# Optimization experiments

Hardware: AMD Instinct MI355X
Metric: run time of the kernel (lower is better)

Reference implementation:

```python
import jax, jax.numpy as jnp
import numpy as np

T_INF = 10
LR_R = 0.02
EPS = 1e-5

def conv(x, w):
    # torch F.conv2d, padding=1, OIHW weights, NCHW data
    return jax.lax.conv_general_dilated(x, w, (1, 1), ((1, 1), (1, 1)),
                                        dimension_numbers=('NCHW', 'OIHW', 'NCHW'))

def convT(x, w):
    # torch ConvTranspose2d (stride=1, padding=1), weight layout (Cin, Cout, kH, kW)
    # equivalent to conv with spatially-flipped, channel-swapped kernel
    wc = jnp.flip(w, (2, 3)).transpose(1, 0, 2, 3)
    return conv(x, wc)

def maxpool2(x):
    return jax.lax.reduce_window(x, -jnp.inf, jax.lax.max, (1, 1, 2, 2), (1, 1, 2, 2), 'VALID')

def avgpool2(x):
    return jax.lax.reduce_window(x, 0.0, jax.lax.add, (1, 1, 2, 2), (1, 1, 2, 2), 'VALID') * 0.25

def bn(x, g, b):
    # BatchNorm2d in training mode (batch statistics, biased variance), eps=1e-5
    m = x.mean((0, 2, 3), keepdims=True)
    v = x.var((0, 2, 3), keepdims=True)
    return (x - m) * jax.lax.rsqrt(v + EPS) * g[None, :, None, None] + b[None, :, None, None]

def up2(x):
    return jnp.repeat(jnp.repeat(x, 2, axis=2), 2, axis=3)

def setup_inputs() -> dict:
    key = jax.random.key(0)
    B, C1, C2, C3 = 256, 64, 128, 256
    ks = jax.random.split(key, 12)
    def w(k, shape, fan_in):
        return jax.random.normal(k, shape, jnp.float32) * (1.0 / np.sqrt(fan_in))
    return {
        'x':  jax.random.normal(ks[0], (B, 3, 32, 32), jnp.float32),
        'W1': w(ks[1], (C1, 3, 3, 3), 3 * 9),
        'W2': w(ks[2], (C2, C1, 3, 3), C1 * 9),
        'W3': w(ks[3], (C3, C2, 3, 3), C2 * 9),
        'P2': w(ks[4], (C2, C1, 3, 3), C2 * 9),  # ConvTranspose2d(C2, C1) weight layout
        'P3': w(ks[5], (C3, C2, 3, 3), C3 * 9),  # ConvTranspose2d(C3, C2) weight layout
        'g1': jnp.ones((C1,), jnp.float32), 'b1': jnp.zeros((C1,), jnp.float32),
        'g2': jnp.ones((C2,), jnp.float32), 'b2': jnp.zeros((C2,), jnp.float32),
        'g3': jnp.ones((C3,), jnp.float32), 'b3': jnp.zeros((C3,), jnp.float32),
    }

def reference(x, W1, W2, W3, P2, P3, g1, b1, g2, b2, g3, b3):
    # feed-forward initialization
    r1 = maxpool2(jax.nn.relu(bn(conv(x, W1), g1, b1)))   # [B,C1,16,16]
    r2 = maxpool2(jax.nn.relu(bn(conv(r1, W2), g2, b2)))  # [B,C2,8,8]
    r3 = maxpool2(jax.nn.relu(bn(conv(r2, W3), g3, b3)))  # [B,C3,4,4]
    # iterative predictive-coding inference
    for _ in range(T_INF):
        pred1 = jnp.tanh(up2(convT(r2, P2)))  # P2(r2) is 8x8, upsample to 16x16
        pred2 = jnp.tanh(up2(convT(r3, P3)))  # P3(r3) is 4x4, upsample to 8x8
        e1 = r1 - pred1
        e2 = r2 - pred2
        dr1 = -e1
        dr2 = -e2 + avgpool2(conv(e1, W2))
        dr3 = avgpool2(conv(e2, W3))
        r1 = jax.nn.relu(r1 + LR_R * dr1)
        r2 = jax.nn.relu(r2 + LR_R * dr2)
        r3 = jax.nn.relu(r3 + LR_R * dr3)
    return (r1, r2, r3)
```

## Files before the change

### kernel.cpp

```cpp
#include <hip/hip_runtime.h>
#include <cstddef>
#include <cstdint>

#define LRr 0.02f

typedef unsigned short u16;
typedef __attribute__((ext_vector_type(8))) __bf16 bf16x8;
typedef __attribute__((ext_vector_type(8))) short short8;
typedef __attribute__((ext_vector_type(4))) float f32x4;
typedef __attribute__((ext_vector_type(4))) u16 u16x4;

static __device__ __forceinline__ u16 f2bf(float f) {
  union { float f; unsigned int u; } v{f};
  unsigned int r = (v.u + 0x7FFFu + ((v.u >> 16) & 1u)) >> 16;
  return (u16)r;
}
static __device__ __forceinline__ float bf2f(u16 h) {
  union { unsigned int u; float f; } v{(unsigned int)h << 16};
  return v.f;
}

static __device__ __forceinline__ void gload_lds16(const void* g, void* l) {
  __builtin_amdgcn_global_load_lds(
      (const __attribute__((address_space(1))) unsigned int*)g,
      (__attribute__((address_space(3))) unsigned int*)l, 16, 0, 0);
}

enum { EP_RAW = 0, EP_E1 = 1, EP_E2 = 2, EP_P2 = 3, EP_P3 = 4 };

template<int H, int CIN, int COUT, int WAVES_M, int WAVES_N, int WN, int NBLK,
         int CS, int IMGS, int EPI, bool STATS>
__device__ __forceinline__ void gemm_body(
    int bid, char* lds,
    const u16* __restrict__ in, const u16* __restrict__ wpk,
    float* __restrict__ fout, u16* __restrict__ bout,
    const u16* __restrict__ aux, float* __restrict__ sums)
{
  constexpr int P = H * H, W = H;
  constexpr int LW = (H == 16) ? 4 : ((H == 8) ? 3 : 2);
  constexpr bool HALO = (IMGS == 1);
  constexpr int MROWS = IMGS * P;
  constexpr int WM = MROWS / WAVES_M;
  constexpr int M_rep = WM / 16, N_rep = WN / 16;
  constexpr int COB = WAVES_N * WN;
  constexpr int PW = H + 2;
  constexpr int ASZ = HALO ? PW * PW * CIN * 2 : MROWS * CIN * 2;
  constexpr int BCH = CS * COB * 2;
  constexpr int CH = CIN / CS;
  constexpr int NS = 9 * CH;
  constexpr int BR = (CS * COB) / 2048;
  static_assert(COB * NBLK == COUT, "n");
  static_assert(WAVES_M * WAVES_N == 4, "w");
  static_assert(ASZ + 2 * BCH <= 65536, "lds");
  static_assert((CS * COB) % 2048 == 0, "br");

  const int tid = threadIdx.x;
  const int l = tid & 63, l15 = l & 15, lq = l >> 4;
  const int wid = tid >> 6;
  const int wn = wid % WAVES_N, wm = wid / WAVES_N;
  const int img0 = (bid / NBLK) * IMGS;
  const int half = bid % NBLK;
  const int co0b = half * COB;
  const int wm0 = wm * WM;
  const int co = co0b + wn * WN;

  auto stageB = [&](int buf, int s) {
    int tap = s / CH, ch = s % CH;
#pragma unroll
    for (int r = 0; r < BR; ++r) {
      int j = r * 256 + tid;
      int ci8 = ch * (CS / 8) + j / COB, c = j % COB;
      const char* gp = (const char*)wpk +
          ((size_t)((tap * (CIN / 8) + ci8) * COUT + co0b + c) << 4);
      char* lp = lds + ASZ + buf * BCH + ((r * 256 + (tid & 192)) << 4);
      gload_lds16(gp, lp);
    }
  };

  stageB(0, 0);
  if constexpr (HALO) {
    for (int i = tid * 16; i < ASZ; i += 4096)
      *(int4*)(lds + i) = make_int4(0, 0, 0, 0);
    __syncthreads();
    constexpr int NCH = P * CIN / 8;
    for (int i = tid; i < NCH; i += 256) {
      int pix = i / (CIN / 8), c8 = i % (CIN / 8);
      const char* gp = (const char*)in + (((size_t)img0 * P + pix) * CIN + c8 * 8) * 2;
      int cell = ((pix >> LW) + 1) * PW + (pix & (W - 1)) + 1;
      int lb = ((cell * CIN + c8 * 8) << 1) ^ ((cell & 7) << 4);
      *(short8*)(lds + lb) = *(const short8*)gp;
    }
  } else {
    constexpr int NCH = MROWS * CIN / 8;
    for (int i = tid; i < NCH; i += 256) {
      int row = i / (CIN / 8), c8 = i % (CIN / 8);
      const char* gp = (const char*)in + ((size_t)img0 * P * CIN + (size_t)i * 8) * 2;
      int lb = ((row * CIN + c8 * 8) << 1) ^ ((row & 7) << 4);
      *(short8*)(lds + lb) = *(const short8*)gp;
    }
  }
  __syncthreads();

  f32x4 acc[M_rep][N_rep];
#pragma unroll
  for (int m = 0; m < M_rep; ++m)
#pragma unroll
    for (int n = 0; n < N_rep; ++n)
#pragma unroll
      for (int r = 0; r < 4; ++r) acc[m][n][r] = 0.f;

  int ym[M_rep], xm[M_rep], imb[M_rep];
#pragma unroll
  for (int m = 0; m < M_rep; ++m) {
    int rb = wm0 + m * 16;
    if constexpr (HALO) {
      int pix = rb + l15;
      ym[m] = pix >> LW;
      xm[m] = pix & (W - 1);
      imb[m] = 0;
    } else {
      imb[m] = rb >> 4;
      ym[m] = l15 >> 2;
      xm[m] = l15 & 3;
    }
  }

  int buf = 0;
  for (int s = 0; s < NS; ++s) {
    const int tap = s / CH, ch = s % CH;
    const int dy = tap / 3, dx = tap % 3;
    if (s + 1 < NS) stageB(buf ^ 1, s + 1);
    int ab[M_rep]; bool av[M_rep];
#pragma unroll
    for (int m = 0; m < M_rep; ++m) {
      if constexpr (HALO) {
        ab[m] = (ym[m] + dy) * PW + xm[m] + dx;
        av[m] = true;
      } else {
        int sy = ym[m] + dy - 1, sx = xm[m] + dx - 1;
        av[m] = ((unsigned)sy < (unsigned)W) & ((unsigned)sx < (unsigned)W);
        ab[m] = imb[m] * P + sy * W + sx;
      }
    }
#pragma unroll
    for (int c2 = 0; c2 < CS / 32; ++c2) {
      const int cc = ch * (CS / 32) + c2;
      bf16x8 af[M_rep], bfr[N_rep];
#pragma unroll
      for (int m = 0; m < M_rep; ++m) {
        int lb = ((ab[m] * CIN + cc * 32 + lq * 8) << 1) ^ ((ab[m] & 7) << 4);
        if constexpr (HALO) {
          af[m] = *(const bf16x8*)(lds + lb);
        } else {
          short8 t{};
          if (av[m]) t = *(const short8*)(lds + lb);
          af[m] = __builtin_bit_cast(bf16x8, t);
        }
      }
#pragma unroll
      for (int n = 0; n < N_rep; ++n)
        bfr[n] = *(const bf16x8*)(lds + ASZ + buf * BCH +
                   (((c2 * 4 + lq) * COB + wn * WN + n * 16 + l15) << 4));
#pragma unroll
      for (int m = 0; m < M_rep; ++m)
#pragma unroll
        for (int n = 0; n < N_rep; ++n)
          acc[m][n] = __builtin_amdgcn_mfma_f32_16x16x32_bf16(af[m], bfr[n], acc[m][n], 0, 0, 0);
    }
    __syncthreads();
    buf ^= 1;
  }

  if constexpr (STATS) {
    float* sbuf = (float*)lds;
    for (int i = tid; i < 2 * COB; i += 256) sbuf[i] = 0.f;
    __syncthreads();
#pragma unroll
    for (int n = 0; n < N_rep; ++n) {
      float s1 = 0.f, s2 = 0.f;
#pragma unroll
      for (int m = 0; m < M_rep; ++m)
#pragma unroll
        for (int r = 0; r < 4; ++r) { float v = acc[m][n][r]; s1 += v; s2 += v * v; }
      s1 += __shfl_xor(s1, 16); s2 += __shfl_xor(s2, 16);
      s1 += __shfl_xor(s1, 32); s2 += __shfl_xor(s2, 32);
      if (lq == 0) {
        int cg = wn * WN + n * 16 + l15;
        atomicAdd(&sbuf[2 * cg], s1);
        atomicAdd(&sbuf[2 * cg + 1], s2);
      }
    }
    __syncthreads();
    for (int i = tid; i < 2 * COB; i += 256) atomicAdd(&sums[2 * co0b + i], sbuf[i]);
  }

  if constexpr (EPI == EP_RAW) {
#pragma unroll
    for (int m = 0; m < M_rep; ++m)
#pragma unroll
      for (int n = 0; n < N_rep; ++n)
#pragma unroll
        for (int r = 0; r < 4; ++r) {
          int pix = wm0 + m * 16 + lq * 4 + r;
          bout[((size_t)img0 * P + pix) * COUT + co + n * 16 + l15] = f2bf(acc[m][n][r]);
        }
  } else if constexpr (EPI == EP_E1) {
#pragma unroll
    for (int m = 0; m < M_rep; ++m)
#pragma unroll
      for (int n = 0; n < N_rep; ++n)
#pragma unroll
        for (int r = 0; r < 4; ++r) {
          int pix = wm0 + m * 16 + lq * 4 + r;
          int y = pix >> 3, x = pix & 7;
          int cg = co + n * 16 + l15;
          float t = tanhf(acc[m][n][r]);
#pragma unroll
          for (int d2 = 0; d2 < 4; ++d2) {
            size_t idx = ((size_t)img0 * 256 + (2 * y + (d2 >> 1)) * 16 + 2 * x + (d2 & 1)) * 64 + cg;
            float rv = fout[idx];
            float e = rv - t;
            bout[idx] = f2bf(e);
            fout[idx] = fmaxf(rv - LRr * e, 0.f);
          }
        }
  } else if constexpr (EPI == EP_E2) {
#pragma unroll
    for (int m = 0; m < M_rep; ++m) {
      const int ime = img0 + imb[m];
#pragma unroll
      for (int n = 0; n < N_rep; ++n)
#pragma unroll
        for (int r = 0; r < 4; ++r) {
          int pix = lq * 4 + r;
          int y = pix >> 2, x = pix & 3;
          int cg = co + n * 16 + l15;
          float t = tanhf(acc[m][n][r]);
#pragma unroll
          for (int d2 = 0; d2 < 4; ++d2) {
            size_t idx = ((size_t)ime * 64 + (2 * y + (d2 >> 1)) * 8 + 2 * x + (d2 & 1)) * 128 + cg;
            bout[idx] = f2bf(fout[idx] - t);
          }
        }
    }
  } else if constexpr (EPI == EP_P2) {
#pragma unroll
    for (int m = 0; m < M_rep; m += 2)
#pragma unroll
      for (int n = 0; n < N_rep; ++n)
#pragma unroll
        for (int r0 = 0; r0 < 4; r0 += 2) {
          float sum = acc[m][n][r0] + acc[m][n][r0 + 1] + acc[m + 1][n][r0] + acc[m + 1][n][r0 + 1];
          int yo = ((wm0 >> 4) + m) >> 1;
          int xo = 2 * lq + (r0 >> 1);
          int cg = co + n * 16 + l15;
          size_t idx = ((size_t)img0 * 64 + yo * 8 + xo) * 128 + cg;
          float old = fout[idx];
          float d = 0.25f * sum - bf2f(aux[idx]);
          float nv = fmaxf(fmaf(LRr, d, old), 0.f);
          fout[idx] = nv;
          bout[idx] = f2bf(nv);
        }
  } else {
#pragma unroll
    for (int m = 0; m < M_rep; ++m)
#pragma unroll
      for (int n = 0; n < N_rep; ++n)
#pragma unroll
        for (int r0 = 0; r0 < 4; r0 += 2) {
          float sx = acc[m][n][r0] + acc[m][n][r0 + 1];
          float sum = sx + __shfl_xor(sx, 32);
          if (l < 32) {
            int yo = (wm0 >> 4) + m;
            int xo = 2 * (lq & 1) + (r0 >> 1);
            int cg = co + n * 16 + l15;
            size_t idx = ((size_t)img0 * 16 + yo * 4 + xo) * 256 + cg;
            float nv = fmaxf(fmaf(LRr, 0.25f * sum, fout[idx]), 0.f);
            fout[idx] = nv;
            bout[idx] = f2bf(nv);
          }
        }
  }
}

__global__ __launch_bounds__(256) void ff2_k(const u16* __restrict__ in, const u16* __restrict__ wpk,
                                             u16* __restrict__ outb, float* __restrict__ sums) {
  __shared__ __align__(16) char lds[57856];
  gemm_body<16, 64, 128, 4, 1, 64, 2, 64, 1, EP_RAW, true>(
      blockIdx.x, lds, in, wpk, nullptr, outb, nullptr, sums);
}

__global__ __launch_bounds__(256) void ff3_k(const u16* __restrict__ in, const u16* __restrict__ wpk,
                                             u16* __restrict__ outb, float* __restrict__ sums) {
  __shared__ __align__(16) char lds[58368];
  gemm_body<8, 128, 256, 2, 2, 64, 2, 64, 1, EP_RAW, true>(
      blockIdx.x, lds, in, wpk, nullptr, outb, nullptr, sums);
}

__global__ __launch_bounds__(256) void ea_k(const u16* __restrict__ r2b, const u16* __restrict__ P2pk,
                                            float* __restrict__ r1, u16* __restrict__ e1b,
                                            const u16* __restrict__ r3b, const u16* __restrict__ P3pk,
                                            const float* __restrict__ r2, u16* __restrict__ e2b) {
  __shared__ __align__(16) char lds[65536];
  if (blockIdx.x < 256)
    gemm_body<8, 128, 64, 2, 2, 32, 1, 128, 1, EP_E1, false>(
        blockIdx.x, lds, r2b, P2pk, r1, e1b, nullptr, nullptr);
  else
    gemm_body<4, 256, 128, 2, 2, 64, 1, 64, 4, EP_E2, false>(
        blockIdx.x - 256, lds, r3b, P3pk, (float*)r2, e2b, nullptr, nullptr);
}

__global__ __launch_bounds__(256) void pb_k(const u16* __restrict__ e1b, const u16* __restrict__ W2pk,
                                            float* __restrict__ r2, u16* __restrict__ r2b,
                                            const u16* __restrict__ e2b, const u16* __restrict__ W3pk,
                                            float* __restrict__ r3, u16* __restrict__ r3b) {
  __shared__ __align__(16) char lds[58368];
  if (blockIdx.x < 512)
    gemm_body<16, 64, 128, 4, 1, 64, 2, 64, 1, EP_P2, false>(
        blockIdx.x, lds, e1b, W2pk, r2, r2b, e2b, nullptr);
  else
    gemm_body<8, 128, 256, 2, 2, 64, 2, 64, 1, EP_P3, false>(
        blockIdx.x - 512, lds, e2b, W3pk, r3, r3b, nullptr, nullptr);
}

template<int CI, int CO, bool FLIP>
__global__ __launch_bounds__(256) void pack_k(const float* __restrict__ src, u16* __restrict__ dst) {
  int idx = blockIdx.x * 256 + threadIdx.x;
  int tap = idx / (CI * CO), rem = idx % (CI * CO);
  int ci = rem / CO, c = rem % CO;
  int dy = tap / 3, dx = tap % 3;
  float v = FLIP ? src[((size_t)ci * CO + c) * 9 + (2 - dy) * 3 + (2 - dx)]
                 : src[((size_t)c * CI + ci) * 9 + dy * 3 + dx];
  dst[(((size_t)tap * (CI / 8) + (ci >> 3)) * CO + c) * 8 + (ci & 7)] = f2bf(v);
}

__global__ void pack1_k(const float* __restrict__ W1, u16* __restrict__ W1pk) {
  for (int j = threadIdx.x; j < 2048; j += 256) {
    int klo = j & 7, rest = j >> 3;
    int co = rest & 63, k8 = rest >> 6;
    int k = k8 * 8 + klo;
    float v = 0.f;
    if (k < 27) {
      int tap = k / 3, cc = k % 3, dy = tap / 3, dx = tap % 3;
      v = W1[((size_t)(co * 3 + cc) * 3 + dy) * 3 + dx];
    }
    W1pk[j] = f2bf(v);
  }
}

template<bool POOL>
__global__ __launch_bounds__(256) void c1_k(const float* __restrict__ x,
                                            const u16* __restrict__ W1pk,
                                            float* __restrict__ sums,
                                            const float* __restrict__ ss,
                                            float* __restrict__ r1,
                                            u16* __restrict__ r1b) {
  __shared__ __align__(16) char lds[28480];
  float* xs = (float*)lds;
  char* Al = lds + 3904;
  char* Bl = lds + 24384;
  const int bid = blockIdx.x;
  const int img = bid >> 2, quad = bid & 3;
  const int ty0 = (quad >> 1) * 16, tx0 = (quad & 1) * 16;
  const int tid = threadIdx.x;
  const int l = tid & 63, l15 = l & 15, lq = l >> 4;
  const int wm = tid >> 6;

  gload_lds16((const char*)W1pk + tid * 16, Bl + ((tid & 192) << 4));
  for (int i = tid; i < 972; i += 256) {
    int xx = i % 18, yy = (i / 18) % 18, cc = i / 324;
    int gy = ty0 + yy - 1, gx = tx0 + xx - 1;
    float v = 0.f;
    if (gy >= 0 && gy < 32 && gx >= 0 && gx < 32)
      v = x[((size_t)(img * 3 + cc) * 32 + gy) * 32 + gx];
    xs[i] = v;
  }
  __syncthreads();
  {
    const int ty = tid >> 4, tx = tid & 15;
#pragma unroll
    for (int i = 0; i < 4; ++i) {
      short8 v{};
#pragma unroll
      for (int j = 0; j < 8; ++j) {
        constexpr int base[4] = {0, 8, 16, 24};
        int k = base[i] + j;
        if (k < 27) {
          int tap = k / 3, cc = k % 3;
          v[j] = (short)f2bf(xs[cc * 324 + (ty + tap / 3) * 18 + tx + tap % 3]);
        }
      }
      *(short8*)(Al + tid * 80 + i * 16) = v;
    }
  }
  __syncthreads();

  f32x4 acc[4][4];
  bf16x8 af[4], bfr[4];
#pragma unroll
  for (int m = 0; m < 4; ++m) {
    int pix = wm * 64 + m * 16 + l15;
    af[m] = *(const bf16x8*)(Al + pix * 80 + lq * 16);
  }
#pragma unroll
  for (int n = 0; n < 4; ++n)
    bfr[n] = *(const bf16x8*)(Bl + ((lq * 64 + n * 16 + l15) << 4));
#pragma unroll
  for (int m = 0; m < 4; ++m)
#pragma unroll
    for (int n = 0; n < 4; ++n) {
      f32x4 z = {0.f, 0.f, 0.f, 0.f};
      acc[m][n] = __builtin_amdgcn_mfma_f32_16x16x32_bf16(af[m], bfr[n], z, 0, 0, 0);
    }

  if constexpr (!POOL) {
    float* sbuf = (float*)lds;
    __syncthreads();
    for (int i = tid; i < 128; i += 256) sbuf[i] = 0.f;
    __syncthreads();
#pragma unroll
    for (int n = 0; n < 4; ++n) {
      float s1 = 0.f, s2 = 0.f;
#pragma unroll
      for (int m = 0; m < 4; ++m)
#pragma unroll
        for (int r = 0; r < 4; ++r) { float v = acc[m][n][r]; s1 += v; s2 += v * v; }
      s1 += __shfl_xor(s1, 16); s2 += __shfl_xor(s2, 16);
      s1 += __shfl_xor(s1, 32); s2 += __shfl_xor(s2, 32);
      if (lq == 0) {
        int cg = n * 16 + l15;
        atomicAdd(&sbuf[2 * cg], s1);
        atomicAdd(&sbuf[2 * cg + 1], s2);
      }
    }
    __syncthreads();
    if (tid < 128) atomicAdd(&sums[tid], sbuf[tid]);
  } else {
    float ssv[4], ssh[4];
#pragma unroll
    for (int n = 0; n < 4; ++n) {
      ssv[n] = ss[n * 16 + l15];
      ssh[n] = ss[64 + n * 16 + l15];
    }
#pragma unroll
    for (int m = 0; m < 4; m += 2)
#pragma unroll
      for (int n = 0; n < 4; ++n)
#pragma unroll
        for (int r0 = 0; r0 < 4; r0 += 2) {
          float a0 = fmaf(acc[m][n][r0], ssv[n], ssh[n]);
          float a1 = fmaf(acc[m][n][r0 + 1], ssv[n], ssh[n]);
          float b0 = fmaf(acc[m + 1][n][r0], ssv[n], ssh[n]);
          float b1 = fmaf(acc[m + 1][n][r0 + 1], ssv[n], ssh[n]);
          float v = fmaxf(fmaxf(fmaxf(a0, a1), fmaxf(b0, b1)), 0.f);
          int py = (ty0 >> 1) + ((wm * 4 + m) >> 1);
          int px = (tx0 >> 1) + ((lq * 4 + r0) >> 1);
          size_t idx = ((size_t)img * 256 + py * 16 + px) * 64 + n * 16 + l15;
          r1[idx] = v;
          r1b[idx] = f2bf(v);
        }
  }
}

__global__ void ss_k(const float* __restrict__ sums, const float* __restrict__ g,
                     const float* __restrict__ b, float* __restrict__ ss, int C, float invN) {
  int c = blockIdx.x * 64 + threadIdx.x;
  if (c < C) {
    float m = sums[2 * c] * invN;
    float var = sums[2 * c + 1] * invN - m * m;
    float sc = g[c] * rsqrtf(var + 1e-5f);
    ss[c] = sc;
    ss[C + c] = b[c] - m * sc;
  }
}

template<int C, int H>
__global__ __launch_bounds__(256) void bnpool_k(const u16* __restrict__ t, const float* __restrict__ ss,
                                                float* __restrict__ r, u16* __restrict__ rb) {
  constexpr int HP = H / 2, C4 = C / 4;
  int idx = blockIdx.x * 256 + threadIdx.x;
  int c4 = idx % C4, po = idx / C4;
  int xo = po % HP, t2 = po / HP;
  int yo = t2 % HP, img = t2 / HP;
  const u16* p0 = t + (((size_t)img * H + 2 * yo) * H + 2 * xo) * C + c4 * 4;
  u16x4 a = *(const u16x4*)p0, b = *(const u16x4*)(p0 + C);
  u16x4 c_ = *(const u16x4*)(p0 + H * C), d = *(const u16x4*)(p0 + H * C + C);
  f32x4 sc = *(const f32x4*)(ss + c4 * 4);
  f32x4 sh = *(const f32x4*)(ss + C + c4 * 4);
  f32x4 o;
#pragma unroll
  for (int j = 0; j < 4; ++j) {
    float v0 = fmaf(bf2f(a[j]), sc[j], sh[j]);
    float v1 = fmaf(bf2f(b[j]), sc[j], sh[j]);
    float v2 = fmaf(bf2f(c_[j]), sc[j], sh[j]);
    float v3 = fmaf(bf2f(d[j]), sc[j], sh[j]);
    o[j] = fmaxf(fmaxf(fmaxf(v0, v1), fmaxf(v2, v3)), 0.f);
  }
  *(f32x4*)(r + (size_t)idx * 4) = o;
  u16x4 ob;
#pragma unroll
  for (int j = 0; j < 4; ++j) ob[j] = f2bf(o[j]);
  *(u16x4*)(rb + (size_t)idx * 4) = ob;
}

template<int P, int C, int CHUNKS>
__global__ __launch_bounds__(256) void tr_k(const float* __restrict__ in, float* __restrict__ out) {
  constexpr int TP = P / CHUNKS;
  __shared__ float tl[TP][C + 1];
  const int img = blockIdx.x, ch = blockIdx.y;
  const float* ip = in + (size_t)img * P * C;
  float* op = out + (size_t)img * P * C;
  for (int i = threadIdx.x; i < TP * C / 4; i += 256) {
    int p = i / (C / 4), c4 = i % (C / 4);
    f32x4 v = *(const f32x4*)&ip[(size_t)(ch * TP + p) * C + c4 * 4];
#pragma unroll
    for (int j = 0; j < 4; ++j) tl[p][c4 * 4 + j] = v[j];
  }
  __syncthreads();
  for (int i = threadIdx.x; i < TP * C; i += 256) {
    int c = i / TP, p = i % TP;
    op[(size_t)c * P + ch * TP + p] = tl[p][c];
  }
}

extern "C" void kernel_launch(void* const* d_in, const int* in_sizes, int n_in,
                              void* d_out, int out_size, void* d_ws, size_t ws_size,
                              hipStream_t stream) {
  const float* x  = (const float*)d_in[0];
  const float* W1 = (const float*)d_in[1];
  const float* W2 = (const float*)d_in[2];
  const float* W3 = (const float*)d_in[3];
  const float* P2 = (const float*)d_in[4];
  const float* P3 = (const float*)d_in[5];
  const float* g1 = (const float*)d_in[6];
  const float* b1 = (const float*)d_in[7];
  const float* g2 = (const float*)d_in[8];
  const float* b2 = (const float*)d_in[9];
  const float* g3 = (const float*)d_in[10];
  const float* b3 = (const float*)d_in[11];

  char* w = (char*)d_ws;
  auto alloc = [&](size_t n) { char* p = w; w += (n + 255) & ~(size_t)255; return p; };
  float* r1  = (float*)alloc(16777216);
  float* r2  = (float*)alloc(8388608);
  float* r3  = (float*)alloc(4194304);
  u16* r1b   = (u16*)alloc(8388608);
  u16* r2b   = (u16*)alloc(4194304);
  u16* r3b   = (u16*)alloc(2097152);
  u16* W2pk  = (u16*)alloc(147456);
  u16* W3pk  = (u16*)alloc(589824);
  u16* P2pk  = (u16*)alloc(147456);
  u16* P3pk  = (u16*)alloc(589824);
  u16* W1pk  = (u16*)alloc(4096);
  float* sums = (float*)alloc(3584);
  float* ssb  = (float*)alloc(3584);
  char* S = alloc(33554432);
  u16* t2 = (u16*)S;
  u16* t3 = (u16*)S;
  u16* e1b = (u16*)S;
  u16* e2b = (u16*)(S + 8388608);

  hipMemsetAsync(sums, 0, 3584, stream);

  pack_k<64, 128, false><<<288, 256, 0, stream>>>(W2, W2pk);
  pack_k<128, 256, false><<<1152, 256, 0, stream>>>(W3, W3pk);
  pack_k<128, 64, true><<<288, 256, 0, stream>>>(P2, P2pk);
  pack_k<256, 128, true><<<1152, 256, 0, stream>>>(P3, P3pk);
  pack1_k<<<1, 256, 0, stream>>>(W1, W1pk);

  c1_k<false><<<1024, 256, 0, stream>>>(x, W1pk, sums, nullptr, nullptr, nullptr);
  ss_k<<<1, 64, 0, stream>>>(sums, g1, b1, ssb, 64, 1.f / 262144.f);
  c1_k<true><<<1024, 256, 0, stream>>>(x, W1pk, nullptr, ssb, r1, r1b);

  ff2_k<<<512, 256, 0, stream>>>(r1b, W2pk, t2, sums + 128);
  ss_k<<<2, 64, 0, stream>>>(sums + 128, g2, b2, ssb + 128, 128, 1.f / 65536.f);
  bnpool_k<128, 16><<<2048, 256, 0, stream>>>(t2, ssb + 128, r2, r2b);

  ff3_k<<<512, 256, 0, stream>>>(r2b, W3pk, t3, sums + 384);
  ss_k<<<4, 64, 0, stream>>>(sums + 384, g3, b3, ssb + 384, 256, 1.f / 16384.f);
  bnpool_k<256, 8><<<1024, 256, 0, stream>>>(t3, ssb + 384, r3, r3b);

  for (int it = 0; it < 10; ++it) {
    ea_k<<<320, 256, 0, stream>>>(r2b, P2pk, r1, e1b, r3b, P3pk, r2, e2b);
    pb_k<<<1024, 256, 0, stream>>>(e1b, W2pk, r2, r2b, e2b, W3pk, r3, r3b);
  }

  float* out = (float*)d_out;
  tr_k<256, 64, 4><<<dim3(256, 4), 256, 0, stream>>>(r1, out);
  tr_k<64, 128, 1><<<dim3(256, 1), 256, 0, stream>>>(r2, out + 4194304);
  tr_k<16, 256, 1><<<dim3(256, 1), 256, 0, stream>>>(r3, out + 6291456);
}
```

Baseline: 794.8 us.

## Preload full weight slab into LDS for conv2 and split pb kernel

For the 16x16 conv (ff2 and the W2 back-projection) the whole 9-tap weight slice for the block's output channels is loaded into LDS once, which removes the per-step double-buffer staging and barriers. The 8x8 W3 convs (ff3 and p3) now process two images per block with a full-CIN chunk, halving the grid and doubling LDS use. The fused pb_k is split into separate p2_k and p3_k launches so each can use its own larger LDS allocation. The larger LDS per block (up to ~115KB) reduces occupancy and adds one launch per iteration.

```diff
diff --git a/kernel.cpp b/kernel.cpp
--- a/kernel.cpp
+++ b/kernel.cpp
@@ -29,7 +29,7 @@
 enum { EP_RAW = 0, EP_E1 = 1, EP_E2 = 2, EP_P2 = 3, EP_P3 = 4 };
 
 template<int H, int CIN, int COUT, int WAVES_M, int WAVES_N, int WN, int NBLK,
-         int CS, int IMGS, int EPI, bool STATS>
+         int CS, int IMGS, int EPI, bool STATS, bool FULLB>
 __device__ __forceinline__ void gemm_body(
     int bid, char* lds,
     const u16* __restrict__ in, const u16* __restrict__ wpk,
@@ -46,13 +46,15 @@
   constexpr int PW = H + 2;
   constexpr int ASZ = HALO ? PW * PW * CIN * 2 : MROWS * CIN * 2;
   constexpr int BCH = CS * COB * 2;
+  constexpr int BSZ = FULLB ? 9 * CIN * COB * 2 : 2 * BCH;
   constexpr int CH = CIN / CS;
   constexpr int NS = 9 * CH;
   constexpr int BR = (CS * COB) / 2048;
   static_assert(COB * NBLK == COUT, "n");
   static_assert(WAVES_M * WAVES_N == 4, "w");
-  static_assert(ASZ + 2 * BCH <= 65536, "lds");
+  static_assert(ASZ + BSZ <= 163840, "lds");
   static_assert((CS * COB) % 2048 == 0, "br");
+  static_assert(!FULLB || CS == CIN, "fb");
 
   const int tid = threadIdx.x;
   const int l = tid & 63, l15 = l & 15, lq = l >> 4;
@@ -77,7 +79,20 @@
     }
   };
 
-  stageB(0, 0);
+  if constexpr (FULLB) {
+    constexpr int TR = (9 * (CIN / 8) * COB) / 256;
+#pragma unroll
+    for (int r = 0; r < TR; ++r) {
+      int j = r * 256 + tid;
+      const char* gp = (const char*)wpk +
+          ((size_t)((j / COB) * COUT + co0b + j % COB) << 4);
+      char* lp = lds + ASZ + ((r * 256 + (tid & 192)) << 4);
+      gload_lds16(gp, lp);
+    }
+  } else {
+    stageB(0, 0);
+  }
+
   if constexpr (HALO) {
     for (int i = tid * 16; i < ASZ; i += 4096)
       *(int4*)(lds + i) = make_int4(0, 0, 0, 0);
@@ -119,9 +134,10 @@
       xm[m] = pix & (W - 1);
       imb[m] = 0;
     } else {
-      imb[m] = rb >> 4;
-      ym[m] = l15 >> 2;
-      xm[m] = l15 & 3;
+      imb[m] = rb / P;
+      int pp = rb % P + l15;
+      ym[m] = pp >> LW;
+      xm[m] = pp & (W - 1);
     }
   }
 
@@ -129,7 +145,9 @@
   for (int s = 0; s < NS; ++s) {
     const int tap = s / CH, ch = s % CH;
     const int dy = tap / 3, dx = tap % 3;
-    if (s + 1 < NS) stageB(buf ^ 1, s + 1);
+    if constexpr (!FULLB) {
+      if (s + 1 < NS) stageB(buf ^ 1, s + 1);
+    }
     int ab[M_rep]; bool av[M_rep];
 #pragma unroll
     for (int m = 0; m < M_rep; ++m) {
@@ -158,21 +176,27 @@
         }
       }
 #pragma unroll
-      for (int n = 0; n < N_rep; ++n)
-        bfr[n] = *(const bf16x8*)(lds + ASZ + buf * BCH +
-                   (((c2 * 4 + lq) * COB + wn * WN + n * 16 + l15) << 4));
+      for (int n = 0; n < N_rep; ++n) {
+        int krow = FULLB ? (tap * (CIN / 8) + c2 * 4 + lq) : (c2 * 4 + lq);
+        int boff = FULLB ? 0 : buf * BCH;
+        bfr[n] = *(const bf16x8*)(lds + ASZ + boff +
+                   ((krow * COB + wn * WN + n * 16 + l15) << 4));
+      }
 #pragma unroll
       for (int m = 0; m < M_rep; ++m)
 #pragma unroll
         for (int n = 0; n < N_rep; ++n)
           acc[m][n] = __builtin_amdgcn_mfma_f32_16x16x32_bf16(af[m], bfr[n], acc[m][n], 0, 0, 0);
     }
-    __syncthreads();
-    buf ^= 1;
+    if constexpr (!FULLB) {
+      __syncthreads();
+      buf ^= 1;
+    }
   }
 
   if constexpr (STATS) {
     float* sbuf = (float*)lds;
+    __syncthreads();
     for (int i = tid; i < 2 * COB; i += 256) sbuf[i] = 0.f;
     __syncthreads();
 #pragma unroll
@@ -263,7 +287,10 @@
         }
   } else {
 #pragma unroll
-    for (int m = 0; m < M_rep; ++m)
+    for (int m = 0; m < M_rep; ++m) {
+      int pb = wm0 + m * 16;
+      int iml = pb / P;
+      int yo = (pb % P) >> 4;
 #pragma unroll
       for (int n = 0; n < N_rep; ++n)
 #pragma unroll
@@ -271,29 +298,29 @@
           float sx = acc[m][n][r0] + acc[m][n][r0 + 1];
           float sum = sx + __shfl_xor(sx, 32);
           if (l < 32) {
-            int yo = (wm0 >> 4) + m;
             int xo = 2 * (lq & 1) + (r0 >> 1);
             int cg = co + n * 16 + l15;
-            size_t idx = ((size_t)img0 * 16 + yo * 4 + xo) * 256 + cg;
+            size_t idx = ((size_t)(img0 + iml) * 16 + yo * 4 + xo) * COUT + cg;
             float nv = fmaxf(fmaf(LRr, 0.25f * sum, fout[idx]), 0.f);
             fout[idx] = nv;
             bout[idx] = f2bf(nv);
           }
         }
+    }
   }
 }
 
 __global__ __launch_bounds__(256) void ff2_k(const u16* __restrict__ in, const u16* __restrict__ wpk,
                                              u16* __restrict__ outb, float* __restrict__ sums) {
-  __shared__ __align__(16) char lds[57856];
-  gemm_body<16, 64, 128, 4, 1, 64, 2, 64, 1, EP_RAW, true>(
+  __shared__ __align__(16) char lds[115200];
+  gemm_body<16, 64, 128, 4, 1, 64, 2, 64, 1, EP_RAW, true, true>(
       blockIdx.x, lds, in, wpk, nullptr, outb, nullptr, sums);
 }
 
 __global__ __launch_bounds__(256) void ff3_k(const u16* __restrict__ in, const u16* __restrict__ wpk,
                                              u16* __restrict__ outb, float* __restrict__ sums) {
-  __shared__ __align__(16) char lds[58368];
-  gemm_body<8, 128, 256, 2, 2, 64, 2, 64, 1, EP_RAW, true>(
+  __shared__ __align__(16) char lds[98304];
+  gemm_body<8, 128, 256, 2, 2, 64, 2, 128, 2, EP_RAW, true, false>(
       blockIdx.x, lds, in, wpk, nullptr, outb, nullptr, sums);
 }
 
@@ -303,24 +330,26 @@
                                             const float* __restrict__ r2, u16* __restrict__ e2b) {
   __shared__ __align__(16) char lds[65536];
   if (blockIdx.x < 256)
-    gemm_body<8, 128, 64, 2, 2, 32, 1, 128, 1, EP_E1, false>(
+    gemm_body<8, 128, 64, 2, 2, 32, 1, 128, 1, EP_E1, false, false>(
         blockIdx.x, lds, r2b, P2pk, r1, e1b, nullptr, nullptr);
   else
-    gemm_body<4, 256, 128, 2, 2, 64, 1, 64, 4, EP_E2, false>(
+    gemm_body<4, 256, 128, 2, 2, 64, 1, 64, 4, EP_E2, false, false>(
         blockIdx.x - 256, lds, r3b, P3pk, (float*)r2, e2b, nullptr, nullptr);
 }
 
-__global__ __launch_bounds__(256) void pb_k(const u16* __restrict__ e1b, const u16* __restrict__ W2pk,
+__global__ __launch_bounds__(256) void p2_k(const u16* __restrict__ e1b, const u16* __restrict__ W2pk,
                                             float* __restrict__ r2, u16* __restrict__ r2b,
-                                            const u16* __restrict__ e2b, const u16* __restrict__ W3pk,
+                                            const u16* __restrict__ e2b) {
+  __shared__ __align__(16) char lds[115200];
+  gemm_body<16, 64, 128, 4, 1, 64, 2, 64, 1, EP_P2, false, true>(
+      blockIdx.x, lds, e1b, W2pk, r2, r2b, e2b, nullptr);
+}
+
+__global__ __launch_bounds__(256) void p3_k(const u16* __restrict__ e2b, const u16* __restrict__ W3pk,
                                             float* __restrict__ r3, u16* __restrict__ r3b) {
-  __shared__ __align__(16) char lds[58368];
-  if (blockIdx.x < 512)
-    gemm_body<16, 64, 128, 4, 1, 64, 2, 64, 1, EP_P2, false>(
-        blockIdx.x, lds, e1b, W2pk, r2, r2b, e2b, nullptr);
-  else
-    gemm_body<8, 128, 256, 2, 2, 64, 2, 64, 1, EP_P3, false>(
-        blockIdx.x - 512, lds, e2b, W3pk, r3, r3b, nullptr, nullptr);
+  __shared__ __align__(16) char lds[98304];
+  gemm_body<8, 128, 256, 2, 2, 64, 2, 128, 2, EP_P3, false, false>(
+      blockIdx.x, lds, e2b, W3pk, r3, r3b, nullptr, nullptr);
 }
 
 template<int CI, int CO, bool FLIP>
@@ -576,13 +605,14 @@
   ss_k<<<2, 64, 0, stream>>>(sums + 128, g2, b2, ssb + 128, 128, 1.f / 65536.f);
   bnpool_k<128, 16><<<2048, 256, 0, stream>>>(t2, ssb + 128, r2, r2b);
 
-  ff3_k<<<512, 256, 0, stream>>>(r2b, W3pk, t3, sums + 384);
+  ff3_k<<<256, 256, 0, stream>>>(r2b, W3pk, t3, sums + 384);
   ss_k<<<4, 64, 0, stream>>>(sums + 384, g3, b3, ssb + 384, 256, 1.f / 16384.f);
   bnpool_k<256, 8><<<1024, 256, 0, stream>>>(t3, ssb + 384, r3, r3b);
 
   for (int it = 0; it < 10; ++it) {
     ea_k<<<320, 256, 0, stream>>>(r2b, P2pk, r1, e1b, r3b, P3pk, r2, e2b);
-    pb_k<<<1024, 256, 0, stream>>>(e1b, W2pk, r2, r2b, e2b, W3pk, r3, r3b);
+    p2_k<<<512, 256, 0, stream>>>(e1b, W2pk, r2, r2b, e2b);
+    p3_k<<<256, 256, 0, stream>>>(e2b, W3pk, r3, r3b);
   }
 
   float* out = (float*)d_out;
```

Result: slower. 884.2 us (+11.2%).

## Triple-buffer weight staging with vmcnt waits, shrink K-chunks, split fused update kernel

Applied to the files above, without the earlier changes.

Weight tiles are now staged two steps ahead into a three-slot ring. Each step waits with explicit s_waitcnt vmcnt plus a single barrier, replacing the old double buffer that needed a trailing __syncthreads every step. K-chunk sizes are halved to cut LDS use, and launch bounds request two or three blocks per CU for more occupancy. The halo/no-halo choice becomes an explicit template flag so the 16x16 conv can skip zero-padded staging. The combined p2/p3 update kernel is split into two launches, which adds launch overhead and removes overlap between the two branches.

```diff
diff --git a/kernel.cpp b/kernel.cpp
--- a/kernel.cpp
+++ b/kernel.cpp
@@ -26,10 +26,18 @@
       (__attribute__((address_space(3))) unsigned int*)l, 16, 0, 0);
 }
 
+template<int N> static __device__ __forceinline__ void wait_vm() {
+  if constexpr (N <= 0)      asm volatile("s_waitcnt vmcnt(0)" ::: "memory");
+  else if constexpr (N == 1) asm volatile("s_waitcnt vmcnt(1)" ::: "memory");
+  else if constexpr (N == 2) asm volatile("s_waitcnt vmcnt(2)" ::: "memory");
+  else if constexpr (N == 3) asm volatile("s_waitcnt vmcnt(3)" ::: "memory");
+  else                       asm volatile("s_waitcnt vmcnt(4)" ::: "memory");
+}
+
 enum { EP_RAW = 0, EP_E1 = 1, EP_E2 = 2, EP_P2 = 3, EP_P3 = 4 };
 
 template<int H, int CIN, int COUT, int WAVES_M, int WAVES_N, int WN, int NBLK,
-         int CS, int IMGS, int EPI, bool STATS>
+         int CS, int IMGS, bool HALO, int EPI, bool STATS>
 __device__ __forceinline__ void gemm_body(
     int bid, char* lds,
     const u16* __restrict__ in, const u16* __restrict__ wpk,
@@ -38,7 +46,6 @@
 {
   constexpr int P = H * H, W = H;
   constexpr int LW = (H == 16) ? 4 : ((H == 8) ? 3 : 2);
-  constexpr bool HALO = (IMGS == 1);
   constexpr int MROWS = IMGS * P;
   constexpr int WM = MROWS / WAVES_M;
   constexpr int M_rep = WM / 16, N_rep = WN / 16;
@@ -49,9 +56,10 @@
   constexpr int CH = CIN / CS;
   constexpr int NS = 9 * CH;
   constexpr int BR = (CS * COB) / 2048;
+  static_assert(!HALO || IMGS == 1, "halo");
   static_assert(COB * NBLK == COUT, "n");
   static_assert(WAVES_M * WAVES_N == 4, "w");
-  static_assert(ASZ + 2 * BCH <= 65536, "lds");
+  static_assert(ASZ + 3 * BCH <= 163840, "lds");
   static_assert((CS * COB) % 2048 == 0, "br");
 
   const int tid = threadIdx.x;
@@ -78,6 +86,8 @@
   };
 
   stageB(0, 0);
+  stageB(1, 1);
+
   if constexpr (HALO) {
     for (int i = tid * 16; i < ASZ; i += 4096)
       *(int4*)(lds + i) = make_int4(0, 0, 0, 0);
@@ -112,24 +122,22 @@
   int ym[M_rep], xm[M_rep], imb[M_rep];
 #pragma unroll
   for (int m = 0; m < M_rep; ++m) {
-    int rb = wm0 + m * 16;
-    if constexpr (HALO) {
-      int pix = rb + l15;
-      ym[m] = pix >> LW;
-      xm[m] = pix & (W - 1);
-      imb[m] = 0;
-    } else {
-      imb[m] = rb >> 4;
-      ym[m] = l15 >> 2;
-      xm[m] = l15 & 3;
-    }
-  }
-
-  int buf = 0;
+    int rb2 = wm0 + m * 16;
+    imb[m] = rb2 / P;
+    int pp = rb2 % P + l15;
+    ym[m] = pp >> LW;
+    xm[m] = pp & (W - 1);
+  }
+
+  int rb = 0;
   for (int s = 0; s < NS; ++s) {
-    const int tap = s / CH, ch = s % CH;
+    const int tap = s / CH;
     const int dy = tap / 3, dx = tap % 3;
-    if (s + 1 < NS) stageB(buf ^ 1, s + 1);
+    if (s + 1 < NS) wait_vm<BR>(); else wait_vm<0>();
+    __builtin_amdgcn_s_barrier();
+    __builtin_amdgcn_sched_barrier(0);
+    if (s + 2 < NS) { int sb = rb + 2; if (sb >= 3) sb -= 3; stageB(sb, s + 2); }
+
     int ab[M_rep]; bool av[M_rep];
 #pragma unroll
     for (int m = 0; m < M_rep; ++m) {
@@ -144,7 +152,7 @@
     }
 #pragma unroll
     for (int c2 = 0; c2 < CS / 32; ++c2) {
-      const int cc = ch * (CS / 32) + c2;
+      const int cc = (s % CH) * (CS / 32) + c2;
       bf16x8 af[M_rep], bfr[N_rep];
 #pragma unroll
       for (int m = 0; m < M_rep; ++m) {
@@ -159,7 +167,7 @@
       }
 #pragma unroll
       for (int n = 0; n < N_rep; ++n)
-        bfr[n] = *(const bf16x8*)(lds + ASZ + buf * BCH +
+        bfr[n] = *(const bf16x8*)(lds + ASZ + rb * BCH +
                    (((c2 * 4 + lq) * COB + wn * WN + n * 16 + l15) << 4));
 #pragma unroll
       for (int m = 0; m < M_rep; ++m)
@@ -167,11 +175,11 @@
         for (int n = 0; n < N_rep; ++n)
           acc[m][n] = __builtin_amdgcn_mfma_f32_16x16x32_bf16(af[m], bfr[n], acc[m][n], 0, 0, 0);
     }
+    rb = (rb == 2) ? 0 : rb + 1;
+  }
+
+  if constexpr (STATS) {
     __syncthreads();
-    buf ^= 1;
-  }
-
-  if constexpr (STATS) {
     float* sbuf = (float*)lds;
     for (int i = tid; i < 2 * COB; i += 256) sbuf[i] = 0.f;
     __syncthreads();
@@ -263,7 +271,10 @@
         }
   } else {
 #pragma unroll
-    for (int m = 0; m < M_rep; ++m)
+    for (int m = 0; m < M_rep; ++m) {
+      int pb = wm0 + m * 16;
+      int iml = pb / P;
+      int yo = (pb % P) >> 4;
 #pragma unroll
       for (int n = 0; n < N_rep; ++n)
 #pragma unroll
@@ -271,56 +282,58 @@
           float sx = acc[m][n][r0] + acc[m][n][r0 + 1];
           float sum = sx + __shfl_xor(sx, 32);
           if (l < 32) {
-            int yo = (wm0 >> 4) + m;
             int xo = 2 * (lq & 1) + (r0 >> 1);
             int cg = co + n * 16 + l15;
-            size_t idx = ((size_t)img0 * 16 + yo * 4 + xo) * 256 + cg;
+            size_t idx = ((size_t)(img0 + iml) * 16 + yo * 4 + xo) * COUT + cg;
             float nv = fmaxf(fmaf(LRr, 0.25f * sum, fout[idx]), 0.f);
             fout[idx] = nv;
             bout[idx] = f2bf(nv);
           }
         }
-  }
-}
-
-__global__ __launch_bounds__(256) void ff2_k(const u16* __restrict__ in, const u16* __restrict__ wpk,
-                                             u16* __restrict__ outb, float* __restrict__ sums) {
-  __shared__ __align__(16) char lds[57856];
-  gemm_body<16, 64, 128, 4, 1, 64, 2, 64, 1, EP_RAW, true>(
+    }
+  }
+}
+
+__global__ __launch_bounds__(256, 3) void ff2_k(const u16* __restrict__ in, const u16* __restrict__ wpk,
+                                                u16* __restrict__ outb, float* __restrict__ sums) {
+  __shared__ __align__(16) char lds[45056];
+  gemm_body<16, 64, 128, 4, 1, 64, 2, 32, 1, false, EP_RAW, true>(
       blockIdx.x, lds, in, wpk, nullptr, outb, nullptr, sums);
 }
 
-__global__ __launch_bounds__(256) void ff3_k(const u16* __restrict__ in, const u16* __restrict__ wpk,
-                                             u16* __restrict__ outb, float* __restrict__ sums) {
-  __shared__ __align__(16) char lds[58368];
-  gemm_body<8, 128, 256, 2, 2, 64, 2, 64, 1, EP_RAW, true>(
+__global__ __launch_bounds__(256, 3) void ff3_k(const u16* __restrict__ in, const u16* __restrict__ wpk,
+                                                u16* __restrict__ outb, float* __restrict__ sums) {
+  __shared__ __align__(16) char lds[50176];
+  gemm_body<8, 128, 256, 2, 2, 64, 2, 32, 1, true, EP_RAW, true>(
       blockIdx.x, lds, in, wpk, nullptr, outb, nullptr, sums);
 }
 
-__global__ __launch_bounds__(256) void ea_k(const u16* __restrict__ r2b, const u16* __restrict__ P2pk,
-                                            float* __restrict__ r1, u16* __restrict__ e1b,
-                                            const u16* __restrict__ r3b, const u16* __restrict__ P3pk,
-                                            const float* __restrict__ r2, u16* __restrict__ e2b) {
-  __shared__ __align__(16) char lds[65536];
+__global__ __launch_bounds__(256, 2) void ea_k(const u16* __restrict__ r2b, const u16* __restrict__ P2pk,
+                                               float* __restrict__ r1, u16* __restrict__ e1b,
+                                               const u16* __restrict__ r3b, const u16* __restrict__ P3pk,
+                                               const float* __restrict__ r2, u16* __restrict__ e2b) {
+  __shared__ __align__(16) char lds[57344];
   if (blockIdx.x < 256)
-    gemm_body<8, 128, 64, 2, 2, 32, 1, 128, 1, EP_E1, false>(
+    gemm_body<8, 128, 64, 2, 2, 32, 1, 64, 1, true, EP_E1, false>(
         blockIdx.x, lds, r2b, P2pk, r1, e1b, nullptr, nullptr);
   else
-    gemm_body<4, 256, 128, 2, 2, 64, 1, 64, 4, EP_E2, false>(
+    gemm_body<4, 256, 128, 2, 2, 64, 1, 32, 4, false, EP_E2, false>(
         blockIdx.x - 256, lds, r3b, P3pk, (float*)r2, e2b, nullptr, nullptr);
 }
 
-__global__ __launch_bounds__(256) void pb_k(const u16* __restrict__ e1b, const u16* __restrict__ W2pk,
-                                            float* __restrict__ r2, u16* __restrict__ r2b,
-                                            const u16* __restrict__ e2b, const u16* __restrict__ W3pk,
-                                            float* __restrict__ r3, u16* __restrict__ r3b) {
-  __shared__ __align__(16) char lds[58368];
-  if (blockIdx.x < 512)
-    gemm_body<16, 64, 128, 4, 1, 64, 2, 64, 1, EP_P2, false>(
-        blockIdx.x, lds, e1b, W2pk, r2, r2b, e2b, nullptr);
-  else
-    gemm_body<8, 128, 256, 2, 2, 64, 2, 64, 1, EP_P3, false>(
-        blockIdx.x - 512, lds, e2b, W3pk, r3, r3b, nullptr, nullptr);
+__global__ __launch_bounds__(256, 3) void p2_k(const u16* __restrict__ e1b, const u16* __restrict__ W2pk,
+                                               float* __restrict__ r2, u16* __restrict__ r2b,
+                                               const u16* __restrict__ e2b) {
+  __shared__ __align__(16) char lds[45056];
+  gemm_body<16, 64, 128, 4, 1, 64, 2, 32, 1, false, EP_P2, false>(
+      blockIdx.x, lds, e1b, W2pk, r2, r2b, e2b, nullptr);
+}
+
+__global__ __launch_bounds__(256, 3) void p3_k(const u16* __restrict__ e2b, const u16* __restrict__ W3pk,
+                                               float* __restrict__ r3, u16* __restrict__ r3b) {
+  __shared__ __align__(16) char lds[50176];
+  gemm_body<8, 128, 256, 2, 2, 64, 2, 32, 1, true, EP_P3, false>(
+      blockIdx.x, lds, e2b, W3pk, r3, r3b, nullptr, nullptr);
 }
 
 template<int CI, int CO, bool FLIP>
@@ -582,7 +595,8 @@
 
   for (int it = 0; it < 10; ++it) {
     ea_k<<<320, 256, 0, stream>>>(r2b, P2pk, r1, e1b, r3b, P3pk, r2, e2b);
-    pb_k<<<1024, 256, 0, stream>>>(e1b, W2pk, r2, r2b, e2b, W3pk, r3, r3b);
+    p2_k<<<512, 256, 0, stream>>>(e1b, W2pk, r2, r2b, e2b);
+    p3_k<<<512, 256, 0, stream>>>(e2b, W3pk, r3, r3b);
   }
 
   float* out = (float*)d_out;
```

Result: slower. 870.6 us (+9.5%).
